# Optimization experiments

Hardware: AMD Instinct MI355X
Metric: run time of the kernel (lower is better)

Reference implementation:

```python
import jax, jax.numpy as jnp
import numpy as np
from jax import lax

B, S, C_IN, D, H, P, W, DFF, K = 32, 4096, 32, 256, 8, 24, 64, 512, 5
DH = D // H
EPS = 1e-5


def _make_starts():
    stride = max(1, W // 2)
    idx = list(range(0, max(S - W + 1, 1), stride))
    if len(idx) == 0 or idx[-1] != S - W:
        if S - W >= 0:
            idx.append(S - W)
    return np.asarray(idx)

STARTS = _make_starts()                      # [M]
WIDX = STARTS[:, None] + np.arange(W)        # [M, W] patch gather indices


def setup_inputs() -> dict:
    key = jax.random.key(0)
    ks = jax.random.split(key, 24)
    r = lambda i, shape, s=0.02: (jax.random.normal(ks[i], shape, jnp.float32) * s)
    return {
        "x": jax.random.normal(ks[0], (B, S, C_IN), jnp.float32),
        "last_close_unused": jnp.zeros((B,), jnp.float32),
        "dw_w": r(1, (C_IN, 1, K), 0.2),      # depthwise conv kernel
        "pw_w": r(2, (D, C_IN), 0.1),         # pointwise conv (1x1)
        "bn_g": jnp.ones((D,), jnp.float32),
        "bn_b": jnp.zeros((D,), jnp.float32),
        "lg_Wq": r(3, (D, D)), "lg_Wk": r(4, (D, D)),
        "lg_Wv": r(5, (D, D)), "lg_Wo": r(6, (D, D)),
        "dec_Qd": r(7, (P, D), 1.0 / np.sqrt(D)),
        "dec_Wq": r(8, (D, D)), "dec_Wk": r(9, (D, D)),
        "dec_Wv": r(10, (D, D)), "dec_Wo": r(11, (D, D)),
        "ff1_w": r(12, (DFF, D)), "ff1_b": jnp.zeros((DFF,), jnp.float32),
        "ff2_w": r(13, (D, DFF)), "ff2_b": jnp.zeros((D,), jnp.float32),
        "out_w": r(14, (1, D)), "out_b": jnp.zeros((1,), jnp.float32),
        "gate_logits": jnp.tile(jnp.array([0.2, 0.4, 0.4], jnp.float32), (P, 1)),
    }


def _ln(x):
    m = x.mean(-1, keepdims=True)
    v = ((x - m) ** 2).mean(-1, keepdims=True)
    return (x - m) / jnp.sqrt(v + EPS)


def _split(t):  # [B, L, D] -> [B, H, L, DH]
    return t.reshape(t.shape[0], -1, H, DH).transpose(0, 2, 1, 3)


def _mha(Q, KV, Wq, Wk, Wv, scale):
    q = _split(Q @ Wq.T)
    k = _split(KV @ Wk.T)
    v = _split(KV @ Wv.T)
    attn = jax.nn.softmax(jnp.einsum('bhqd,bhkd->bhqk', q, k) * scale, axis=-1)
    o = jnp.einsum('bhqk,bhkd->bhqd', attn, v)
    o = o.transpose(0, 2, 1, 3).reshape(Q.shape[0], -1, D)
    return o, attn


def reference(x, last_close_unused, dw_w, pw_w, bn_g, bn_b,
              lg_Wq, lg_Wk, lg_Wv, lg_Wo,
              dec_Qd, dec_Wq, dec_Wk, dec_Wv, dec_Wo,
              ff1_w, ff1_b, ff2_w, ff2_b, out_w, out_b, gate_logits):
    # --- DepthwisePointwise front-end ---
    xt = jnp.transpose(x, (0, 2, 1))                         # [B, C, S]
    z = lax.conv_general_dilated(xt, dw_w, (1,), [(K // 2, K // 2)],
                                 dimension_numbers=('NCH', 'OIH', 'NCH'),
                                 feature_group_count=C_IN)
    z = jnp.einsum('dc,bcs->bds', pw_w, z)                   # pointwise 1x1
    z = jax.nn.gelu(z, approximate=False)
    m = z.mean((0, 2), keepdims=True)                        # BatchNorm1d (batch stats)
    v = ((z - m) ** 2).mean((0, 2), keepdims=True)
    z = (z - m) / jnp.sqrt(v + EPS) * bn_g[None, :, None] + bn_b[None, :, None]
    z = jnp.transpose(z, (0, 2, 1))                          # [B, S, D]

    # --- LocalGlobalAttention: patch-mean queries over full sequence K/V ---
    Q = z[:, WIDX].mean(axis=2)                              # [B, M, D]
    scale = 1.0 / np.sqrt(DH)
    o, attn_g = _mha(Q, z, lg_Wq, lg_Wk, lg_Wv, scale)
    Hh = _ln(o @ lg_Wo.T + Q)                                # [B, M, D]

    # --- CrossDecoder: learned queries ---
    Qd = jnp.broadcast_to(dec_Qd[None], (B, P, D))
    o2, attn_d = _mha(Qd, Hh, dec_Wq, dec_Wk, dec_Wv, scale)
    z2 = _ln(o2 @ dec_Wo.T + Qd)
    u = jax.nn.gelu(z2 @ ff1_w.T + ff1_b, approximate=False)
    u = _ln(u @ ff2_w.T + ff2_b + z2)
    y_global = (u @ out_w.T + out_b)[..., 0]                 # [B, P]

    # --- Gated combine: residual=0, local=global ---
    g = jax.nn.softmax(gate_logits, axis=-1)                 # [P, 3]
    y = g[:, 1][None, :] * y_global + g[:, 2][None, :] * y_global
    return (y, attn_g, attn_d)
```

## Files before the change

kernel.cpp:

```cpp
#include <hip/hip_runtime.h>
#include <hip/hip_bf16.h>
#include <cmath>

typedef unsigned short u16;
typedef __attribute__((ext_vector_type(4))) float f32x4;
typedef __attribute__((ext_vector_type(8))) short s16x8;

__device__ __forceinline__ float b2f(u16 u) { return __uint_as_float(((unsigned)u) << 16); }
__device__ __forceinline__ u16 f2b(float f) {
    unsigned u = __float_as_uint(f);
    unsigned r = (u + 0x7fffu + ((u >> 16) & 1u)) >> 16;
    return (u16)r;
}
__device__ __forceinline__ float gelu_f(float x) {
    float t = x * (0.7978845608f + 0.0356774081f * x * x);
    float e = exp2f(2.885390082f * t);
    return 0.5f * x * (1.0f + (e - 1.0f) / (e + 1.0f));
}

#define FOLD 0.25503590f

__global__ __launch_bounds__(256) void prep0_k(const float* __restrict__ pw_w,
        const float* __restrict__ lg_Wq, const float* __restrict__ lg_Wo,
        const float* __restrict__ dec_Wk, const float* __restrict__ dec_Wv,
        const float* __restrict__ dec_Wo, const float* __restrict__ ff1_w,
        const float* __restrict__ ff2_w,
        u16* __restrict__ pwb, u16* __restrict__ Wq_b, u16* __restrict__ Wo_b,
        u16* __restrict__ Wk2_b, u16* __restrict__ Wv2_b, u16* __restrict__ Wo2b,
        u16* __restrict__ ff1b, u16* __restrict__ ff2b)
{
    int idx = blockIdx.x * 256 + threadIdx.x;
    if (idx < 327680) {
        int which = idx >> 16, r = idx & 65535;
        const float* srcs[5] = {lg_Wq, lg_Wo, dec_Wk, dec_Wv, dec_Wo};
        u16* dsts[5] = {Wq_b, Wo_b, Wk2_b, Wv2_b, Wo2b};
        dsts[which][r] = f2b(srcs[which][r]);
    } else if (idx < 458752) {
        int r = idx - 327680;
        ff1b[r] = f2b(ff1_w[r]);
    } else if (idx < 589824) {
        int r = idx - 458752;
        ff2b[r] = f2b(ff2_w[r]);
    } else {
        int r = idx - 589824;
        pwb[r] = f2b(pw_w[r]);
    }
}

__global__ __launch_bounds__(256) void dwpw_k(const float* __restrict__ x,
        const float* __restrict__ dw_w, const u16* __restrict__ pwb,
        u16* __restrict__ zp, float* __restrict__ csum, float* __restrict__ csum2)
{
    __shared__ float xs[68][33];
    __shared__ __align__(16) u16 As[64][40];
    const int t = threadIdx.x;
    const int b = blockIdx.x >> 6, s0 = (blockIdx.x & 63) << 6;
    const int r0 = blockIdx.x * 64;
    const int lane = t & 63, w = t >> 6;
    const int l16 = lane & 15, hi = lane >> 4;

    for (int idx = t; idx < 68 * 32; idx += 256) {
        int row = idx >> 5, c = idx & 31;
        int sg = s0 - 2 + row;
        xs[row][c] = (sg >= 0 && sg < 4096) ? x[((size_t)b * 4096 + sg) * 32 + c] : 0.0f;
    }
    const int cc = t & 31;
    float wv[5];
    #pragma unroll
    for (int k = 0; k < 5; ++k) wv[k] = dw_w[cc * 5 + k];
    __syncthreads();
    #pragma unroll
    for (int i = 0; i < 8; ++i) {
        int sl = (t + i * 256) >> 5;
        float acc = 0;
        #pragma unroll
        for (int k = 0; k < 5; ++k) acc += xs[sl + k][cc] * wv[k];
        As[sl][cc] = f2b(acc);
    }
    __syncthreads();

    const int n0 = w * 64;
    f32x4 zero = {0, 0, 0, 0};
    s16x8 bf[4];
    #pragma unroll
    for (int ni = 0; ni < 4; ++ni)
        bf[ni] = *(const s16x8*)(pwb + (n0 + ni * 16 + l16) * 32 + hi * 8);

    float cl[4] = {0,0,0,0}, ch[4] = {0,0,0,0};
    float ql[4] = {0,0,0,0}, qh[4] = {0,0,0,0};

    #pragma unroll
    for (int mi = 0; mi < 4; ++mi) {
        s16x8 af = *(const s16x8*)&As[mi * 16 + l16][hi * 8];
        #pragma unroll
        for (int ni = 0; ni < 4; ++ni) {
            f32x4 acc = __builtin_amdgcn_mfma_f32_16x16x32_bf16(af, bf[ni], zero, 0, 0, 0);
            int col = n0 + ni * 16 + l16;
            int rowb = r0 + mi * 16 + hi * 4;
            #pragma unroll
            for (int r = 0; r < 4; ++r) {
                float e = gelu_f(acc[r]);
                zp[(size_t)(rowb + r) * 256 + col] = f2b(e);
                if (mi < 2) { cl[ni] += e; ql[ni] += e * e; }
                else        { ch[ni] += e; qh[ni] += e * e; }
            }
        }
    }
    #pragma unroll
    for (int ni = 0; ni < 4; ++ni) {
        #pragma unroll
        for (int m = 16; m <= 32; m <<= 1) {
            cl[ni] += __shfl_xor(cl[ni], m);
            ch[ni] += __shfl_xor(ch[ni], m);
            ql[ni] += __shfl_xor(ql[ni], m);
            qh[ni] += __shfl_xor(qh[ni], m);
        }
        if (lane < 16) {
            int col = n0 + ni * 16 + lane;
            size_t bc = (size_t)(r0 >> 5);
            csum [bc * 256 + col]       = cl[ni];
            csum [(bc + 1) * 256 + col] = ch[ni];
            csum2[bc * 256 + col]       = ql[ni];
            csum2[(bc + 1) * 256 + col] = qh[ni];
        }
    }
}

__global__ __launch_bounds__(256) void stats2_k(const float* __restrict__ csum,
        const float* __restrict__ csum2, float* __restrict__ statp)
{
    int j = blockIdx.x, t = threadIdx.x;
    float s1 = 0, s2 = 0;
    for (int i = 0; i < 64; ++i) {
        s1 += csum [(size_t)(j * 64 + i) * 256 + t];
        s2 += csum2[(size_t)(j * 64 + i) * 256 + t];
    }
    statp[j * 512 + t] = s1;
    statp[j * 512 + 256 + t] = s2;
}

__global__ __launch_bounds__(256) void prep1_k(const float* __restrict__ statp,
        const float* __restrict__ bn_g, const float* __restrict__ bn_b,
        const float* __restrict__ gate_logits,
        float* __restrict__ a_ws, float* __restrict__ c_ws, float* __restrict__ coef)
{
    int t = threadIdx.x;
    float s1 = 0, s2 = 0;
    for (int j = 0; j < 64; ++j) {
        s1 += statp[j * 512 + t];
        s2 += statp[j * 512 + 256 + t];
    }
    const float invN = 1.0f / 131072.0f;
    float mean = s1 * invN;
    float var = s2 * invN - mean * mean;
    float av = bn_g[t] * rsqrtf(var + 1e-5f);
    a_ws[t] = av;
    c_ws[t] = bn_b[t] - mean * av;
    if (t < 24) {
        float g0 = gate_logits[t * 3], g1 = gate_logits[t * 3 + 1], g2 = gate_logits[t * 3 + 2];
        float mx = fmaxf(g0, fmaxf(g1, g2));
        float e0 = __expf(g0 - mx), e1 = __expf(g1 - mx), e2 = __expf(g2 - mx);
        coef[t] = (e1 + e2) / (e0 + e1 + e2);
    }
}

__global__ __launch_bounds__(256) void prepx_k(const float* __restrict__ lg_Wk,
        const float* __restrict__ lg_Wv, const float* __restrict__ a_ws,
        const float* __restrict__ c_ws, const float* __restrict__ dec_Qd,
        const float* __restrict__ dec_Wq, const float* __restrict__ csum,
        const u16* __restrict__ Wq_b,
        u16* __restrict__ Wk_b, u16* __restrict__ Wv_b,
        float* __restrict__ betak, float* __restrict__ betav,
        float* __restrict__ q2, u16* __restrict__ qb)
{
    __shared__ __align__(16) char sm[41728];
    const int bid = blockIdx.x, t = threadIdx.x;
    if (bid < 512) {
        float* red = (float*)sm;
        int which = bid >> 8, row = bid & 255;
        const float* Wsrc = which ? lg_Wv : lg_Wk;
        float wv = Wsrc[row * 256 + t];
        (which ? Wv_b : Wk_b)[row * 256 + t] = f2b(wv * a_ws[t]);
        float v = wv * c_ws[t];
        for (int m = 32; m; m >>= 1) v += __shfl_xor(v, m);
        if ((t & 63) == 0) red[t >> 6] = v;
        __syncthreads();
        if (t == 0) (which ? betav : betak)[row] = red[0] + red[1] + red[2] + red[3];
    } else if (bid < 528) {
        float (*wq)[260] = (float(*)[260])sm;
        float (*qd)[260] = (float(*)[260])(sm + 16640);
        int j = bid - 512;
        for (int idx = t; idx < 4096; idx += 256) {
            int tl = idx >> 8, d = idx & 255;
            wq[tl][d] = dec_Wq[(j * 16 + tl) * 256 + d];
        }
        for (int idx = t; idx < 6144; idx += 256) {
            int p = idx >> 8, d = idx & 255;
            qd[p][d] = dec_Qd[idx];
        }
        __syncthreads();
        for (int o = t; o < 384; o += 256) {
            int p = o >> 4, tl = o & 15;
            float s = 0;
            #pragma unroll 8
            for (int d = 0; d < 256; ++d) s += qd[p][d] * wq[tl][d];
            q2[p * 256 + j * 16 + tl] = s;
        }
    } else {
        u16* As = (u16*)sm;
        float* aa = (float*)(sm + 32768);
        float* ccx = (float*)(sm + 33792);
        const int r0 = (bid - 528) * 64;
        const int lane = t & 63, w = t >> 6;
        const int l16 = lane & 15, hi = lane >> 4;
        aa[t] = a_ws[t] * 0.015625f;
        ccx[t] = c_ws[t];
        __syncthreads();
        #pragma unroll
        for (int i = 0; i < 8; ++i) {
            int c = t + i * 256;
            int row = c >> 5, c16 = c & 31;
            int g = r0 + row, mm = g & 127;
            u16 tmp[8];
            if (mm == 127) {
                #pragma unroll
                for (int j = 0; j < 8; ++j) tmp[j] = 0;
            } else {
                const float* c0p = csum + (size_t)g * 256 + c16 * 8;
                const float* c1p = c0p + 256;
                #pragma unroll
                for (int j = 0; j < 8; ++j) {
                    int d = c16 * 8 + j;
                    tmp[j] = f2b((c0p[j] + c1p[j]) * aa[d] + ccx[d]);
                }
            }
            int boff = (c16 * 16) ^ ((row & 7) << 4);
            *(s16x8*)((char*)As + row * 512 + boff) = *(s16x8*)tmp;
        }
        __syncthreads();
        const int n0 = w * 64;
        f32x4 zero = {0, 0, 0, 0};
        f32x4 acc[4][4];
        #pragma unroll
        for (int mi = 0; mi < 4; ++mi)
            #pragma unroll
            for (int ni = 0; ni < 4; ++ni) acc[mi][ni] = zero;
        #pragma unroll
        for (int kk = 0; kk < 8; ++kk) {
            s16x8 af[4], bf[4];
            #pragma unroll
            for (int mi = 0; mi < 4; ++mi) {
                int row = mi * 16 + l16;
                int boff = (kk * 64 + hi * 16) ^ ((row & 7) << 4);
                af[mi] = *(const s16x8*)((const char*)As + row * 512 + boff);
            }
            #pragma unroll
            for (int ni = 0; ni < 4; ++ni)
                bf[ni] = *(const s16x8*)(Wq_b + (n0 + ni * 16 + l16) * 256 + kk * 32 + hi * 8);
            #pragma unroll
            for (int mi = 0; mi < 4; ++mi)
                #pragma unroll
                for (int ni = 0; ni < 4; ++ni)
                    acc[mi][ni] = __builtin_amdgcn_mfma_f32_16x16x32_bf16(af[mi], bf[ni], acc[mi][ni], 0, 0, 0);
        }
        #pragma unroll
        for (int mi = 0; mi < 4; ++mi)
            #pragma unroll
            for (int ni = 0; ni < 4; ++ni) {
                int col = n0 + ni * 16 + l16;
                int rowb = r0 + mi * 16 + hi * 4;
                #pragma unroll
                for (int r = 0; r < 4; ++r)
                    qb[(size_t)(rowb + r) * 256 + col] = f2b(acc[mi][ni][r] * FOLD);
            }
    }
}

__global__ __launch_bounds__(256) void kv_k(const u16* __restrict__ zp,
        const u16* __restrict__ Wk, const u16* __restrict__ Wv,
        const float* __restrict__ betak, const float* __restrict__ betav,
        u16* __restrict__ kb, u16* __restrict__ vT)
{
    __shared__ __align__(16) char smem[36864];
    const int t = threadIdx.x;
    const int r0 = blockIdx.x * 64;
    const int lane = t & 63, w = t >> 6;
    const int l16 = lane & 15, hi = lane >> 4;

    const u16* Ag = zp + (size_t)r0 * 256;
    #pragma unroll
    for (int i = 0; i < 8; ++i) {
        int c = t + i * 256;
        int row = c >> 5, c16 = c & 31;
        s16x8 v = *(const s16x8*)(Ag + row * 256 + c16 * 8);
        int boff = (c16 * 16) ^ ((row & 7) << 4);
        *(s16x8*)(smem + row * 512 + boff) = v;
    }
    __syncthreads();

    const int n0 = w * 64;
    f32x4 zero = {0, 0, 0, 0};
    f32x4 acc[4][4];
    #pragma unroll
    for (int mi = 0; mi < 4; ++mi)
        #pragma unroll
        for (int ni = 0; ni < 4; ++ni) acc[mi][ni] = zero;

    #pragma unroll
    for (int kk = 0; kk < 8; ++kk) {
        s16x8 af[4], bfk[4];
        #pragma unroll
        for (int mi = 0; mi < 4; ++mi) {
            int row = mi * 16 + l16;
            int boff = (kk * 64 + hi * 16) ^ ((row & 7) << 4);
            af[mi] = *(const s16x8*)(smem + row * 512 + boff);
        }
        #pragma unroll
        for (int ni = 0; ni < 4; ++ni)
            bfk[ni] = *(const s16x8*)(Wk + (n0 + ni * 16 + l16) * 256 + kk * 32 + hi * 8);
        #pragma unroll
        for (int mi = 0; mi < 4; ++mi)
            #pragma unroll
            for (int ni = 0; ni < 4; ++ni)
                acc[mi][ni] = __builtin_amdgcn_mfma_f32_16x16x32_bf16(af[mi], bfk[ni], acc[mi][ni], 0, 0, 0);
    }
    #pragma unroll
    for (int mi = 0; mi < 4; ++mi)
        #pragma unroll
        for (int ni = 0; ni < 4; ++ni) {
            int col = n0 + ni * 16 + l16;
            float bv = betak[col];
            int rowb = r0 + mi * 16 + hi * 4;
            #pragma unroll
            for (int r = 0; r < 4; ++r)
                kb[(size_t)(rowb + r) * 256 + col] = f2b(acc[mi][ni][r] + bv);
        }

    #pragma unroll
    for (int mi = 0; mi < 4; ++mi)
        #pragma unroll
        for (int ni = 0; ni < 4; ++ni) acc[mi][ni] = zero;
    #pragma unroll
    for (int kk = 0; kk < 8; ++kk) {
        s16x8 af[4], bfv[4];
        #pragma unroll
        for (int mi = 0; mi < 4; ++mi) {
            int row = mi * 16 + l16;
            int boff = (kk * 64 + hi * 16) ^ ((row & 7) << 4);
            af[mi] = *(const s16x8*)(smem + row * 512 + boff);
        }
        #pragma unroll
        for (int ni = 0; ni < 4; ++ni)
            bfv[ni] = *(const s16x8*)(Wv + (n0 + ni * 16 + l16) * 256 + kk * 32 + hi * 8);
        #pragma unroll
        for (int mi = 0; mi < 4; ++mi)
            #pragma unroll
            for (int ni = 0; ni < 4; ++ni)
                acc[mi][ni] = __builtin_amdgcn_mfma_f32_16x16x32_bf16(af[mi], bfv[ni], acc[mi][ni], 0, 0, 0);
    }
    __syncthreads();
    #pragma unroll
    for (int mi = 0; mi < 4; ++mi)
        #pragma unroll
        for (int ni = 0; ni < 4; ++ni) {
            int col = n0 + ni * 16 + l16;
            float bv = betav[col];
            int rowb = mi * 16 + hi * 4;
            ushort4 pk;
            pk.x = f2b(acc[mi][ni][0] + bv);
            pk.y = f2b(acc[mi][ni][1] + bv);
            pk.z = f2b(acc[mi][ni][2] + bv);
            pk.w = f2b(acc[mi][ni][3] + bv);
            char* p = smem + col * 144 + ((((rowb >> 3) ^ (col & 7)) & 7) << 4) + ((rowb & 7) << 1);
            *(ushort4*)p = pk;
        }
    __syncthreads();
    const int b = r0 >> 12;
    const int sblk = (r0 & 4095) >> 6;
    u16* vout = vT + (size_t)(b * 8) * 131072 + (size_t)sblk * 2048;
    #pragma unroll
    for (int j = 0; j < 8; ++j) {
        int gid = j * 256 + t;
        int col = gid >> 3, oct = gid & 7;
        const char* p = smem + col * 144 + (((oct ^ (col & 7)) & 7) << 4);
        s16x8 v = *(const s16x8*)p;
        int h = col >> 5, dh = col & 31;
        *(s16x8*)(vout + (size_t)h * 131072 + dh * 64 + oct * 8) = v;
    }
}

template<int MODE>
__global__ __launch_bounds__(256) void gemm_g(const u16* __restrict__ A,
        const u16* __restrict__ W, const float* __restrict__ bias,
        void* __restrict__ Cout, int K, int ntn)
{
    __shared__ u16 As[64 * 256];
    const int t = threadIdx.x;
    const int rt = blockIdx.x / ntn, nt = blockIdx.x % ntn;
    const int r0 = rt * 64, N = ntn * 256;
    const int lane = t & 63, w = t >> 6;
    const int l16 = lane & 15, hi = lane >> 4;

    const u16* Ag = A + (size_t)r0 * K;
    const int n0 = w * 64;
    f32x4 zero = {0, 0, 0, 0};
    f32x4 acc[4][4];
    #pragma unroll
    for (int mi = 0; mi < 4; ++mi)
        #pragma unroll
        for (int ni = 0; ni < 4; ++ni) acc[mi][ni] = zero;

    for (int kc = 0; kc < K; kc += 256) {
        if (kc) __syncthreads();
        #pragma unroll
        for (int i = 0; i < 8; ++i) {
            int c = t + i * 256;
            int row = c >> 5, c16 = c & 31;
            s16x8 v = *(const s16x8*)(Ag + (size_t)row * K + kc + c16 * 8);
            int boff = (c16 * 16) ^ ((row & 7) << 4);
            *(s16x8*)((char*)As + row * 512 + boff) = v;
        }
        __syncthreads();
        #pragma unroll
        for (int kk = 0; kk < 8; ++kk) {
            s16x8 af[4], bf[4];
            #pragma unroll
            for (int mi = 0; mi < 4; ++mi) {
                int row = mi * 16 + l16;
                int boff = (kk * 64 + hi * 16) ^ ((row & 7) << 4);
                af[mi] = *(const s16x8*)((const char*)As + row * 512 + boff);
            }
            #pragma unroll
            for (int ni = 0; ni < 4; ++ni) {
                int j = nt * 256 + n0 + ni * 16 + l16;
                bf[ni] = *(const s16x8*)(W + (size_t)j * K + kc + kk * 32 + hi * 8);
            }
            #pragma unroll
            for (int mi = 0; mi < 4; ++mi)
                #pragma unroll
                for (int ni = 0; ni < 4; ++ni)
                    acc[mi][ni] = __builtin_amdgcn_mfma_f32_16x16x32_bf16(af[mi], bf[ni], acc[mi][ni], 0, 0, 0);
        }
    }

    #pragma unroll
    for (int mi = 0; mi < 4; ++mi)
        #pragma unroll
        for (int ni = 0; ni < 4; ++ni) {
            int col = nt * 256 + n0 + ni * 16 + l16;
            float bv = bias ? bias[col] : 0.0f;
            int rowb = r0 + mi * 16 + hi * 4;
            #pragma unroll
            for (int r = 0; r < 4; ++r) {
                float v = acc[mi][ni][r] + bv;
                if (MODE == 0)      ((u16*)Cout)[(size_t)(rowb + r) * N + col] = f2b(v);
                else if (MODE == 1) ((float*)Cout)[(size_t)(rowb + r) * N + col] = v;
                else                ((u16*)Cout)[(size_t)(rowb + r) * N + col] = f2b(gelu_f(v));
            }
        }
}

__global__ __launch_bounds__(256) void gemm_dual(const u16* __restrict__ A,
        const u16* __restrict__ W0, const u16* __restrict__ W1,
        u16* __restrict__ C0, u16* __restrict__ C1)
{
    __shared__ u16 As[64 * 256];
    const int t = threadIdx.x;
    const int which = blockIdx.x >> 6;
    const int r0 = (blockIdx.x & 63) * 64;
    const u16* W = which ? W1 : W0;
    u16* C = which ? C1 : C0;
    const int lane = t & 63, w = t >> 6;
    const int l16 = lane & 15, hi = lane >> 4;

    const u16* Ag = A + (size_t)r0 * 256;
    #pragma unroll
    for (int i = 0; i < 8; ++i) {
        int c = t + i * 256;
        int row = c >> 5, c16 = c & 31;
        s16x8 v = *(const s16x8*)(Ag + row * 256 + c16 * 8);
        int boff = (c16 * 16) ^ ((row & 7) << 4);
        *(s16x8*)((char*)As + row * 512 + boff) = v;
    }
    __syncthreads();

    const int n0 = w * 64;
    f32x4 zero = {0, 0, 0, 0};
    f32x4 acc[4][4];
    #pragma unroll
    for (int mi = 0; mi < 4; ++mi)
        #pragma unroll
        for (int ni = 0; ni < 4; ++ni) acc[mi][ni] = zero;

    #pragma unroll
    for (int kk = 0; kk < 8; ++kk) {
        s16x8 af[4], bf[4];
        #pragma unroll
        for (int mi = 0; mi < 4; ++mi) {
            int row = mi * 16 + l16;
            int boff = (kk * 64 + hi * 16) ^ ((row & 7) << 4);
            af[mi] = *(const s16x8*)((const char*)As + row * 512 + boff);
        }
        #pragma unroll
        for (int ni = 0; ni < 4; ++ni)
            bf[ni] = *(const s16x8*)(W + (n0 + ni * 16 + l16) * 256 + kk * 32 + hi * 8);
        #pragma unroll
        for (int mi = 0; mi < 4; ++mi)
            #pragma unroll
            for (int ni = 0; ni < 4; ++ni)
                acc[mi][ni] = __builtin_amdgcn_mfma_f32_16x16x32_bf16(af[mi], bf[ni], acc[mi][ni], 0, 0, 0);
    }
    #pragma unroll
    for (int mi = 0; mi < 4; ++mi)
        #pragma unroll
        for (int ni = 0; ni < 4; ++ni) {
            int col = n0 + ni * 16 + l16;
            int rowb = r0 + mi * 16 + hi * 4;
            #pragma unroll
            for (int r = 0; r < 4; ++r)
                C[(size_t)(rowb + r) * 256 + col] = f2b(acc[mi][ni][r]);
        }
}

__global__ __launch_bounds__(512) void attn_k(const u16* __restrict__ qb,
        const u16* __restrict__ kb, const u16* __restrict__ vT,
        u16* __restrict__ ob, float* __restrict__ attn_out)
{
    const int b = blockIdx.x >> 3, h = blockIdx.x & 7;
    const int t = threadIdx.x, w = t >> 6, lane = t & 63;
    const int l16 = lane & 15, hi = lane >> 4;

    __shared__ u16 p_lds[8][16][48];
    __shared__ float buf[8][16][68];

    s16x8 qf = *(const s16x8*)(qb + ((size_t)(b * 128 + w * 16 + l16)) * 256 + h * 32 + hi * 8);
    const u16* kbase = kb + (size_t)b * 4096 * 256 + h * 32 + hi * 8;
    const u16* vbase = vT + (size_t)(b * 8 + h) * 131072 + hi * 8;

    float dacc[4] = {0, 0, 0, 0};
    f32x4 zero = {0, 0, 0, 0};
    f32x4 oacc[2]; oacc[0] = zero; oacc[1] = zero;

    s16x8 kf0 = *(const s16x8*)(kbase + (size_t)l16 * 256);
    s16x8 kf1 = *(const s16x8*)(kbase + (size_t)(16 + l16) * 256);
    s16x8 vf0 = *(const s16x8*)(vbase + l16 * 64);
    s16x8 vf1 = *(const s16x8*)(vbase + (16 + l16) * 64);

    for (int s0 = 0; s0 < 4096; s0 += 32) {
        s16x8 k0 = kf0, k1 = kf1, v0 = vf0, v1 = vf1;
        int sn = s0 + 32;
        if (sn < 4096) {
            kf0 = *(const s16x8*)(kbase + (size_t)(sn + l16) * 256);
            kf1 = *(const s16x8*)(kbase + (size_t)(sn + 16 + l16) * 256);
            vf0 = *(const s16x8*)(vbase + (sn >> 6) * 2048 + l16 * 64 + (sn & 63));
            vf1 = *(const s16x8*)(vbase + (sn >> 6) * 2048 + (16 + l16) * 64 + (sn & 63));
        }
        f32x4 lg0 = __builtin_amdgcn_mfma_f32_16x16x32_bf16(qf, k0, zero, 0, 0, 0);
        f32x4 lg1 = __builtin_amdgcn_mfma_f32_16x16x32_bf16(qf, k1, zero, 0, 0, 0);
        #pragma unroll
        for (int r = 0; r < 4; ++r) {
            float e0 = exp2f(lg0[r]);
            float e1 = exp2f(lg1[r]);
            dacc[r] += e0 + e1;
            p_lds[w][hi * 4 + r][l16] = f2b(e0);
            p_lds[w][hi * 4 + r][16 + l16] = f2b(e1);
        }
        s16x8 pf = *(const s16x8*)(&p_lds[w][l16][hi * 8]);
        oacc[0] = __builtin_amdgcn_mfma_f32_16x16x32_bf16(pf, v0, oacc[0], 0, 0, 0);
        oacc[1] = __builtin_amdgcn_mfma_f32_16x16x32_bf16(pf, v1, oacc[1], 0, 0, 0);
    }

    #pragma unroll
    for (int m = 1; m <= 8; m <<= 1) {
        #pragma unroll
        for (int r = 0; r < 4; ++r) dacc[r] += __shfl_xor(dacc[r], m);
    }
    float rinv[4];
    #pragma unroll
    for (int r = 0; r < 4; ++r) rinv[r] = 1.0f / dacc[r];

    #pragma unroll
    for (int vi = 0; vi < 2; ++vi)
        #pragma unroll
        for (int r = 0; r < 4; ++r) {
            int mg = w * 16 + hi * 4 + r;
            ob[(size_t)(b * 128 + mg) * 256 + h * 32 + vi * 16 + l16] = f2b(oacc[vi][r] * rinv[r]);
        }

    float* ab = attn_out + (size_t)(b * 8 + h) * 127 * 4096;
    const int srow = lane >> 4;
    const int scol = (lane & 15) * 4;

    for (int s0 = 0; s0 < 4096; s0 += 64) {
        #pragma unroll
        for (int kk = 0; kk < 4; ++kk) {
            int sg = s0 + kk * 16 + l16;
            s16x8 kf = *(const s16x8*)(kbase + (size_t)sg * 256);
            f32x4 lg = __builtin_amdgcn_mfma_f32_16x16x32_bf16(qf, kf, zero, 0, 0, 0);
            #pragma unroll
            for (int r = 0; r < 4; ++r)
                buf[w][hi * 4 + r][kk * 16 + l16] = exp2f(lg[r]) * rinv[r];
        }
        #pragma unroll
        for (int rb = 0; rb < 4; ++rb) {
            int row = rb * 4 + srow;
            int mg = w * 16 + row;
            f32x4 v = *(const f32x4*)&buf[w][row][scol];
            if (mg < 127)
                *(f32x4*)(ab + (size_t)mg * 4096 + s0 + scol) = v;
        }
    }
}

__global__ __launch_bounds__(256) void gemm_lnhh(const u16* __restrict__ A,
        const u16* __restrict__ W, const float* __restrict__ csum,
        const float* __restrict__ a_ws, const float* __restrict__ c_ws,
        u16* __restrict__ Hb)
{
    __shared__ __align__(16) char sm[67584];
    __shared__ float aa[256], cc2[256];
    float (*Cs)[264] = (float(*)[264])sm;
    const int t = threadIdx.x;
    const int r0 = blockIdx.x * 64;
    const int lane = t & 63, w = t >> 6;
    const int l16 = lane & 15, hi = lane >> 4;

    aa[t] = a_ws[t] * 0.015625f;
    cc2[t] = c_ws[t];

    const u16* Ag = A + (size_t)r0 * 256;
    #pragma unroll
    for (int i = 0; i < 8; ++i) {
        int c = t + i * 256;
        int row = c >> 5, c16 = c & 31;
        s16x8 v = *(const s16x8*)(Ag + row * 256 + c16 * 8);
        int boff = (c16 * 16) ^ ((row & 7) << 4);
        *(s16x8*)(sm + row * 512 + boff) = v;
    }
    __syncthreads();

    const int n0 = w * 64;
    f32x4 zero = {0, 0, 0, 0};
    f32x4 acc[4][4];
    #pragma unroll
    for (int mi = 0; mi < 4; ++mi)
        #pragma unroll
        for (int ni = 0; ni < 4; ++ni) acc[mi][ni] = zero;
    #pragma unroll
    for (int kk = 0; kk < 8; ++kk) {
        s16x8 af[4], bf[4];
        #pragma unroll
        for (int mi = 0; mi < 4; ++mi) {
            int row = mi * 16 + l16;
            int boff = (kk * 64 + hi * 16) ^ ((row & 7) << 4);
            af[mi] = *(const s16x8*)(sm + row * 512 + boff);
        }
        #pragma unroll
        for (int ni = 0; ni < 4; ++ni)
            bf[ni] = *(const s16x8*)(W + (n0 + ni * 16 + l16) * 256 + kk * 32 + hi * 8);
        #pragma unroll
        for (int mi = 0; mi < 4; ++mi)
            #pragma unroll
            for (int ni = 0; ni < 4; ++ni)
                acc[mi][ni] = __builtin_amdgcn_mfma_f32_16x16x32_bf16(af[mi], bf[ni], acc[mi][ni], 0, 0, 0);
    }
    __syncthreads();
    #pragma unroll
    for (int mi = 0; mi < 4; ++mi)
        #pragma unroll
        for (int ni = 0; ni < 4; ++ni) {
            int col = n0 + ni * 16 + l16;
            int rowb = mi * 16 + hi * 4;
            #pragma unroll
            for (int r = 0; r < 4; ++r)
                Cs[rowb + r][col] = acc[mi][ni][r];
        }
    __syncthreads();
    for (int pass = 0; pass < 16; ++pass) {
        int row = pass * 4 + w;
        int g = r0 + row, mm = g & 127;
        float v[4];
        #pragma unroll
        for (int j = 0; j < 4; ++j) {
            int d = lane + j * 64;
            float qv = 0.0f;
            if (mm != 127)
                qv = (csum[(size_t)g * 256 + d] + csum[(size_t)(g + 1) * 256 + d]) * aa[d] + cc2[d];
            v[j] = Cs[row][d] + qv;
        }
        float s = v[0] + v[1] + v[2] + v[3];
        for (int m = 32; m; m >>= 1) s += __shfl_xor(s, m);
        float mean = s * (1.0f / 256.0f);
        float q = 0;
        #pragma unroll
        for (int j = 0; j < 4; ++j) { float d_ = v[j] - mean; q += d_ * d_; }
        for (int m = 32; m; m >>= 1) q += __shfl_xor(q, m);
        float rs = rsqrtf(q * (1.0f / 256.0f) + 1e-5f);
        #pragma unroll
        for (int j = 0; j < 4; ++j)
            Hb[(size_t)g * 256 + lane + j * 64] = f2b((v[j] - mean) * rs);
    }
}

__global__ __launch_bounds__(256) void dec_attn_k(const float* __restrict__ q2,
        const u16* __restrict__ k2b, const u16* __restrict__ v2b,
        float* __restrict__ attn_d, u16* __restrict__ o2b)
{
    __shared__ float qs2[24 * 32];
    __shared__ float ks[128][33];
    __shared__ float vs[128][33];
    __shared__ float lg2[24 * 128];
    __shared__ float sinv[24];
    int bid = blockIdx.x, b = bid >> 3, h = bid & 7;
    int t = threadIdx.x;
    const float scale = 0.17677669529663687f;
    for (int idx = t; idx < 4096; idx += 256) {
        int row = idx >> 5, c = idx & 31;
        ks[row][c] = b2f(k2b[((size_t)(b * 128 + row)) * 256 + h * 32 + c]);
        vs[row][c] = b2f(v2b[((size_t)(b * 128 + row)) * 256 + h * 32 + c]);
    }
    for (int idx = t; idx < 768; idx += 256) {
        int p = idx >> 5, i = idx & 31;
        qs2[idx] = q2[p * 256 + h * 32 + i];
    }
    __syncthreads();
    for (int idx = t; idx < 3048; idx += 256) {
        int p = idx / 127, m = idx - p * 127;
        float s = 0;
        #pragma unroll 8
        for (int i = 0; i < 32; ++i) s += qs2[p * 32 + i] * ks[m][i];
        lg2[p * 128 + m] = __expf(s * scale);
    }
    __syncthreads();
    if (t < 24) {
        float s = 0;
        for (int m = 0; m < 127; ++m) s += lg2[t * 128 + m];
        sinv[t] = 1.0f / s;
    }
    __syncthreads();
    float* ad = attn_d + (size_t)bid * 24 * 127;
    for (int idx = t; idx < 3048; idx += 256) {
        int p = idx / 127, m = idx - p * 127;
        float av = lg2[p * 128 + m] * sinv[p];
        lg2[p * 128 + m] = av;
        ad[idx] = av;
    }
    __syncthreads();
    for (int idx = t; idx < 768; idx += 256) {
        int p = idx >> 5, dh = idx & 31;
        float s = 0;
        for (int m = 0; m < 127; ++m)
            s += lg2[p * 128 + m] * vs[m][dh];
        o2b[((size_t)(b * 24 + p)) * 256 + h * 32 + dh] = f2b(s);
    }
}

__global__ __launch_bounds__(256) void gemm_ln3(const u16* __restrict__ A,
        const u16* __restrict__ W, const float* __restrict__ dec_Qd,
        float* __restrict__ z2f, u16* __restrict__ z2b)
{
    __shared__ __align__(16) char sm[67584];
    float (*Cs)[264] = (float(*)[264])sm;
    const int t = threadIdx.x;
    const int r0 = blockIdx.x * 64;
    const int lane = t & 63, w = t >> 6;
    const int l16 = lane & 15, hi = lane >> 4;

    const u16* Ag = A + (size_t)r0 * 256;
    #pragma unroll
    for (int i = 0; i < 8; ++i) {
        int c = t + i * 256;
        int row = c >> 5, c16 = c & 31;
        s16x8 v = *(const s16x8*)(Ag + row * 256 + c16 * 8);
        int boff = (c16 * 16) ^ ((row & 7) << 4);
        *(s16x8*)(sm + row * 512 + boff) = v;
    }
    __syncthreads();

    const int n0 = w * 64;
    f32x4 zero = {0, 0, 0, 0};
    f32x4 acc[4][4];
    #pragma unroll
    for (int mi = 0; mi < 4; ++mi)
        #pragma unroll
        for (int ni = 0; ni < 4; ++ni) acc[mi][ni] = zero;
    #pragma unroll
    for (int kk = 0; kk < 8; ++kk) {
        s16x8 af[4], bf[4];
        #pragma unroll
        for (int mi = 0; mi < 4; ++mi) {
            int row = mi * 16 + l16;
            int boff = (kk * 64 + hi * 16) ^ ((row & 7) << 4);
            af[mi] = *(const s16x8*)(sm + row * 512 + boff);
        }
        #pragma unroll
        for (int ni = 0; ni < 4; ++ni)
            bf[ni] = *(const s16x8*)(W + (n0 + ni * 16 + l16) * 256 + kk * 32 + hi * 8);
        #pragma unroll
        for (int mi = 0; mi < 4; ++mi)
            #pragma unroll
            for (int ni = 0; ni < 4; ++ni)
                acc[mi][ni] = __builtin_amdgcn_mfma_f32_16x16x32_bf16(af[mi], bf[ni], acc[mi][ni], 0, 0, 0);
    }
    __syncthreads();
    #pragma unroll
    for (int mi = 0; mi < 4; ++mi)
        #pragma unroll
        for (int ni = 0; ni < 4; ++ni) {
            int col = n0 + ni * 16 + l16;
            int rowb = mi * 16 + hi * 4;
            #pragma unroll
            for (int r = 0; r < 4; ++r)
                Cs[rowb + r][col] = acc[mi][ni][r];
        }
    __syncthreads();
    for (int pass = 0; pass < 16; ++pass) {
        int row = pass * 4 + w;
        int g = r0 + row, p = g % 24;
        float v[4];
        #pragma unroll
        for (int j = 0; j < 4; ++j) {
            int d = lane + j * 64;
            v[j] = Cs[row][d] + dec_Qd[p * 256 + d];
        }
        float s = v[0] + v[1] + v[2] + v[3];
        for (int m = 32; m; m >>= 1) s += __shfl_xor(s, m);
        float mean = s * (1.0f / 256.0f);
        float q = 0;
        #pragma unroll
        for (int j = 0; j < 4; ++j) { float d_ = v[j] - mean; q += d_ * d_; }
        for (int m = 32; m; m >>= 1) q += __shfl_xor(q, m);
        float rs = rsqrtf(q * (1.0f / 256.0f) + 1e-5f);
        #pragma unroll
        for (int j = 0; j < 4; ++j) {
            float u = (v[j] - mean) * rs;
            z2f[(size_t)g * 256 + lane + j * 64] = u;
            z2b[(size_t)g * 256 + lane + j * 64] = f2b(u);
        }
    }
}

__global__ __launch_bounds__(256) void gemm_ln5(const u16* __restrict__ A,
        const u16* __restrict__ W, const float* __restrict__ bias,
        const float* __restrict__ z2f, const float* __restrict__ out_w,
        const float* __restrict__ out_b, const float* __restrict__ coef,
        float* __restrict__ y)
{
    __shared__ __align__(16) char sm[67584];
    float (*Cs)[264] = (float(*)[264])sm;
    const int t = threadIdx.x;
    const int r0 = blockIdx.x * 64;
    const int lane = t & 63, w = t >> 6;
    const int l16 = lane & 15, hi = lane >> 4;
    const int K = 512;

    const u16* Ag = A + (size_t)r0 * K;
    const int n0 = w * 64;
    f32x4 zero = {0, 0, 0, 0};
    f32x4 acc[4][4];
    #pragma unroll
    for (int mi = 0; mi < 4; ++mi)
        #pragma unroll
        for (int ni = 0; ni < 4; ++ni) acc[mi][ni] = zero;

    for (int kc = 0; kc < K; kc += 256) {
        if (kc) __syncthreads();
        #pragma unroll
        for (int i = 0; i < 8; ++i) {
            int c = t + i * 256;
            int row = c >> 5, c16 = c & 31;
            s16x8 v = *(const s16x8*)(Ag + (size_t)row * K + kc + c16 * 8);
            int boff = (c16 * 16) ^ ((row & 7) << 4);
            *(s16x8*)(sm + row * 512 + boff) = v;
        }
        __syncthreads();
        #pragma unroll
        for (int kk = 0; kk < 8; ++kk) {
            s16x8 af[4], bf[4];
            #pragma unroll
            for (int mi = 0; mi < 4; ++mi) {
                int row = mi * 16 + l16;
                int boff = (kk * 64 + hi * 16) ^ ((row & 7) << 4);
                af[mi] = *(const s16x8*)(sm + row * 512 + boff);
            }
            #pragma unroll
            for (int ni = 0; ni < 4; ++ni)
                bf[ni] = *(const s16x8*)(W + (size_t)(n0 + ni * 16 + l16) * K + kc + kk * 32 + hi * 8);
            #pragma unroll
            for (int mi = 0; mi < 4; ++mi)
                #pragma unroll
                for (int ni = 0; ni < 4; ++ni)
                    acc[mi][ni] = __builtin_amdgcn_mfma_f32_16x16x32_bf16(af[mi], bf[ni], acc[mi][ni], 0, 0, 0);
        }
    }
    __syncthreads();
    #pragma unroll
    for (int mi = 0; mi < 4; ++mi)
        #pragma unroll
        for (int ni = 0; ni < 4; ++ni) {
            int col = n0 + ni * 16 + l16;
            int rowb = mi * 16 + hi * 4;
            #pragma unroll
            for (int r = 0; r < 4; ++r)
                Cs[rowb + r][col] = acc[mi][ni][r];
        }
    __syncthreads();
    for (int pass = 0; pass < 16; ++pass) {
        int row = pass * 4 + w;
        int g = r0 + row, p = g % 24;
        float v[4];
        #pragma unroll
        for (int j = 0; j < 4; ++j) {
            int d = lane + j * 64;
            v[j] = Cs[row][d] + bias[d] + z2f[(size_t)g * 256 + d];
        }
        float s = v[0] + v[1] + v[2] + v[3];
        for (int m = 32; m; m >>= 1) s += __shfl_xor(s, m);
        float mean = s * (1.0f / 256.0f);
        float q = 0;
        #pragma unroll
        for (int j = 0; j < 4; ++j) { float d_ = v[j] - mean; q += d_ * d_; }
        for (int m = 32; m; m >>= 1) q += __shfl_xor(q, m);
        float rs = rsqrtf(q * (1.0f / 256.0f) + 1e-5f);
        float yp = 0;
        #pragma unroll
        for (int j = 0; j < 4; ++j)
            yp += (v[j] - mean) * rs * out_w[lane + j * 64];
        for (int m = 32; m; m >>= 1) yp += __shfl_xor(yp, m);
        if (lane == 0)
            y[g] = coef[p] * (yp + out_b[0]);
    }
}

extern "C" void kernel_launch(void* const* d_in, const int* in_sizes, int n_in,
                              void* d_out, int out_size, void* d_ws, size_t ws_size,
                              hipStream_t stream)
{
    const float* x        = (const float*)d_in[0];
    const float* dw_w     = (const float*)d_in[2];
    const float* pw_w     = (const float*)d_in[3];
    const float* bn_g     = (const float*)d_in[4];
    const float* bn_b     = (const float*)d_in[5];
    const float* lg_Wq    = (const float*)d_in[6];
    const float* lg_Wk    = (const float*)d_in[7];
    const float* lg_Wv    = (const float*)d_in[8];
    const float* lg_Wo    = (const float*)d_in[9];
    const float* dec_Qd   = (const float*)d_in[10];
    const float* dec_Wq   = (const float*)d_in[11];
    const float* dec_Wk   = (const float*)d_in[12];
    const float* dec_Wv   = (const float*)d_in[13];
    const float* dec_Wo   = (const float*)d_in[14];
    const float* ff1_w    = (const float*)d_in[15];
    const float* ff1_b    = (const float*)d_in[16];
    const float* ff2_w    = (const float*)d_in[17];
    const float* ff2_b    = (const float*)d_in[18];
    const float* out_w    = (const float*)d_in[19];
    const float* out_b    = (const float*)d_in[20];
    const float* gate_lg  = (const float*)d_in[21];

    char* ws = (char*)d_ws;
    size_t off = 0;
    auto alloc = [&](size_t bytes) -> void* {
        void* p = ws + off;
        off = (off + bytes + 255) & ~(size_t)255;
        return p;
    };
    u16*   zp    = (u16*)  alloc(67108864);
    u16*   kb    = (u16*)  alloc(67108864);
    u16*   vT    = (u16*)  alloc(67108864);
    float* csum  = (float*)alloc(4194304);
    float* csum2 = (float*)alloc(4194304);
    u16*   qb    = (u16*)  alloc(2097152);
    u16*   ob    = (u16*)  alloc(2097152);
    u16*   Hb    = (u16*)  alloc(2097152);
    u16*   k2b   = (u16*)  alloc(2097152);
    u16*   v2b   = (u16*)  alloc(2097152);
    u16*   o2b   = (u16*)  alloc(393216);
    float* z2f   = (float*)alloc(786432);
    u16*   z2b   = (u16*)  alloc(393216);
    u16*   u1b   = (u16*)  alloc(786432);
    float* q2    = (float*)alloc(24576);
    float* statp = (float*)alloc(131072);
    float* a_ws  = (float*)alloc(1024);
    float* c_ws  = (float*)alloc(1024);
    float* betak = (float*)alloc(1024);
    float* betav = (float*)alloc(1024);
    float* coef  = (float*)alloc(256);
    u16*   pwb   = (u16*)  alloc(16384);
    u16*   Wk_b  = (u16*)  alloc(131072);
    u16*   Wv_b  = (u16*)  alloc(131072);
    u16*   Wq_b  = (u16*)  alloc(131072);
    u16*   Wo_b  = (u16*)  alloc(131072);
    u16*   Wk2_b = (u16*)  alloc(131072);
    u16*   Wv2_b = (u16*)  alloc(131072);
    u16*   Wo2b  = (u16*)  alloc(131072);
    u16*   ff1b  = (u16*)  alloc(262144);
    u16*   ff2b  = (u16*)  alloc(262144);

    float* y_out  = (float*)d_out;
    float* attn_g = y_out + 768;
    float* attn_d = attn_g + (size_t)32 * 8 * 127 * 4096;

    prep0_k<<<2336, 256, 0, stream>>>(pw_w, lg_Wq, lg_Wo, dec_Wk, dec_Wv, dec_Wo, ff1_w, ff2_w,
                                      pwb, Wq_b, Wo_b, Wk2_b, Wv2_b, Wo2b, ff1b, ff2b);
    dwpw_k<<<2048, 256, 0, stream>>>(x, dw_w, pwb, zp, csum, csum2);
    stats2_k<<<64, 256, 0, stream>>>(csum, csum2, statp);
    prep1_k<<<1, 256, 0, stream>>>(statp, bn_g, bn_b, gate_lg, a_ws, c_ws, coef);
    prepx_k<<<592, 256, 0, stream>>>(lg_Wk, lg_Wv, a_ws, c_ws, dec_Qd, dec_Wq, csum, Wq_b,
                                     Wk_b, Wv_b, betak, betav, q2, qb);
    kv_k<<<2048, 256, 0, stream>>>(zp, Wk_b, Wv_b, betak, betav, kb, vT);
    attn_k<<<256, 512, 0, stream>>>(qb, kb, vT, ob, attn_g);
    gemm_lnhh<<<64, 256, 0, stream>>>(ob, Wo_b, csum, a_ws, c_ws, Hb);
    gemm_dual<<<128, 256, 0, stream>>>(Hb, Wk2_b, Wv2_b, k2b, v2b);
    dec_attn_k<<<256, 256, 0, stream>>>(q2, k2b, v2b, attn_d, o2b);
    gemm_ln3<<<12, 256, 0, stream>>>(o2b, Wo2b, dec_Qd, z2f, z2b);
    gemm_g<2><<<24, 256, 0, stream>>>(z2b, ff1b, ff1_b, u1b, 256, 2);
    gemm_ln5<<<12, 256, 0, stream>>>(u1b, ff2b, ff2_b, z2f, out_w, out_b, coef, y_out);
}
```

Measured before the change: 579.9 us.

## Split attention key range across two waves per query group with LDS reduction

```diff
diff --git a/kernel.cpp b/kernel.cpp
--- a/kernel.cpp
+++ b/kernel.cpp
@@ -522,18 +522,19 @@
         }
 }
 
-__global__ __launch_bounds__(512) void attn_k(const u16* __restrict__ qb,
+__global__ __launch_bounds__(1024) void attn_k(const u16* __restrict__ qb,
         const u16* __restrict__ kb, const u16* __restrict__ vT,
         u16* __restrict__ ob, float* __restrict__ attn_out)
 {
+    __shared__ __align__(16) char sm[36864];
     const int b = blockIdx.x >> 3, h = blockIdx.x & 7;
     const int t = threadIdx.x, w = t >> 6, lane = t & 63;
+    const int qg = w >> 1, sh = w & 1;
     const int l16 = lane & 15, hi = lane >> 4;
 
-    __shared__ u16 p_lds[8][16][48];
-    __shared__ float buf[8][16][68];
-
-    s16x8 qf = *(const s16x8*)(qb + ((size_t)(b * 128 + w * 16 + l16)) * 256 + h * 32 + hi * 8);
+    u16* p_lds = (u16*)sm + w * 768;
+
+    s16x8 qf = *(const s16x8*)(qb + ((size_t)(b * 128 + qg * 16 + l16)) * 256 + h * 32 + hi * 8);
     const u16* kbase = kb + (size_t)b * 4096 * 256 + h * 32 + hi * 8;
     const u16* vbase = vT + (size_t)(b * 8 + h) * 131072 + hi * 8;
 
@@ -541,15 +542,16 @@
     f32x4 zero = {0, 0, 0, 0};
     f32x4 oacc[2]; oacc[0] = zero; oacc[1] = zero;
 
-    s16x8 kf0 = *(const s16x8*)(kbase + (size_t)l16 * 256);
-    s16x8 kf1 = *(const s16x8*)(kbase + (size_t)(16 + l16) * 256);
-    s16x8 vf0 = *(const s16x8*)(vbase + l16 * 64);
-    s16x8 vf1 = *(const s16x8*)(vbase + (16 + l16) * 64);
-
-    for (int s0 = 0; s0 < 4096; s0 += 32) {
+    const int sbeg = sh * 2048, send = sbeg + 2048;
+    s16x8 kf0 = *(const s16x8*)(kbase + (size_t)(sbeg + l16) * 256);
+    s16x8 kf1 = *(const s16x8*)(kbase + (size_t)(sbeg + 16 + l16) * 256);
+    s16x8 vf0 = *(const s16x8*)(vbase + (sbeg >> 6) * 2048 + l16 * 64 + (sbeg & 63));
+    s16x8 vf1 = *(const s16x8*)(vbase + (sbeg >> 6) * 2048 + (16 + l16) * 64 + (sbeg & 63));
+
+    for (int s0 = sbeg; s0 < send; s0 += 32) {
         s16x8 k0 = kf0, k1 = kf1, v0 = vf0, v1 = vf1;
         int sn = s0 + 32;
-        if (sn < 4096) {
+        if (sn < send) {
             kf0 = *(const s16x8*)(kbase + (size_t)(sn + l16) * 256);
             kf1 = *(const s16x8*)(kbase + (size_t)(sn + 16 + l16) * 256);
             vf0 = *(const s16x8*)(vbase + (sn >> 6) * 2048 + l16 * 64 + (sn & 63));
@@ -562,10 +564,10 @@
             float e0 = exp2f(lg0[r]);
             float e1 = exp2f(lg1[r]);
             dacc[r] += e0 + e1;
-            p_lds[w][hi * 4 + r][l16] = f2b(e0);
-            p_lds[w][hi * 4 + r][16 + l16] = f2b(e1);
-        }
-        s16x8 pf = *(const s16x8*)(&p_lds[w][l16][hi * 8]);
+            p_lds[(hi * 4 + r) * 48 + l16] = f2b(e0);
+            p_lds[(hi * 4 + r) * 48 + 16 + l16] = f2b(e1);
+        }
+        s16x8 pf = *(const s16x8*)(p_lds + l16 * 48 + hi * 8);
         oacc[0] = __builtin_amdgcn_mfma_f32_16x16x32_bf16(pf, v0, oacc[0], 0, 0, 0);
         oacc[1] = __builtin_amdgcn_mfma_f32_16x16x32_bf16(pf, v1, oacc[1], 0, 0, 0);
     }
@@ -575,37 +577,57 @@
         #pragma unroll
         for (int r = 0; r < 4; ++r) dacc[r] += __shfl_xor(dacc[r], m);
     }
+
+    __syncthreads();
+    float* op = (float*)sm;
+    float* den_s = (float*)(sm + 32768);
+    #pragma unroll
+    for (int vi = 0; vi < 2; ++vi)
+        #pragma unroll
+        for (int r = 0; r < 4; ++r)
+            op[((w * 16 + hi * 4 + r) * 32) + vi * 16 + l16] = oacc[vi][r];
+    if (l16 == 0) {
+        #pragma unroll
+        for (int r = 0; r < 4; ++r) den_s[w * 16 + hi * 4 + r] = dacc[r];
+    }
+    __syncthreads();
     float rinv[4];
     #pragma unroll
-    for (int r = 0; r < 4; ++r) rinv[r] = 1.0f / dacc[r];
-
-    #pragma unroll
-    for (int vi = 0; vi < 2; ++vi)
-        #pragma unroll
-        for (int r = 0; r < 4; ++r) {
-            int mg = w * 16 + hi * 4 + r;
-            ob[(size_t)(b * 128 + mg) * 256 + h * 32 + vi * 16 + l16] = f2b(oacc[vi][r] * rinv[r]);
-        }
-
+    for (int r = 0; r < 4; ++r)
+        rinv[r] = 1.0f / (dacc[r] + den_s[(w ^ 1) * 16 + hi * 4 + r]);
+
+    if (sh == 0) {
+        #pragma unroll
+        for (int vi = 0; vi < 2; ++vi)
+            #pragma unroll
+            for (int r = 0; r < 4; ++r) {
+                int mg = qg * 16 + hi * 4 + r;
+                float o = oacc[vi][r] + op[(((w ^ 1) * 16 + hi * 4 + r) * 32) + vi * 16 + l16];
+                ob[(size_t)(b * 128 + mg) * 256 + h * 32 + vi * 16 + l16] = f2b(o * rinv[r]);
+            }
+    }
+    __syncthreads();
+
+    float* bw = (float*)sm + w * 16 * 36;
     float* ab = attn_out + (size_t)(b * 8 + h) * 127 * 4096;
-    const int srow = lane >> 4;
-    const int scol = (lane & 15) * 4;
-
-    for (int s0 = 0; s0 < 4096; s0 += 64) {
-        #pragma unroll
-        for (int kk = 0; kk < 4; ++kk) {
+    const int srow = lane >> 3;
+    const int scol = (lane & 7) * 4;
+
+    for (int s0 = sbeg; s0 < send; s0 += 32) {
+        #pragma unroll
+        for (int kk = 0; kk < 2; ++kk) {
             int sg = s0 + kk * 16 + l16;
             s16x8 kf = *(const s16x8*)(kbase + (size_t)sg * 256);
             f32x4 lg = __builtin_amdgcn_mfma_f32_16x16x32_bf16(qf, kf, zero, 0, 0, 0);
             #pragma unroll
             for (int r = 0; r < 4; ++r)
-                buf[w][hi * 4 + r][kk * 16 + l16] = exp2f(lg[r]) * rinv[r];
-        }
-        #pragma unroll
-        for (int rb = 0; rb < 4; ++rb) {
-            int row = rb * 4 + srow;
-            int mg = w * 16 + row;
-            f32x4 v = *(const f32x4*)&buf[w][row][scol];
+                bw[(hi * 4 + r) * 36 + kk * 16 + l16] = exp2f(lg[r]) * rinv[r];
+        }
+        #pragma unroll
+        for (int rb = 0; rb < 2; ++rb) {
+            int row = rb * 8 + srow;
+            int mg = qg * 16 + row;
+            f32x4 v = *(const f32x4*)(bw + row * 36 + scol);
             if (mg < 127)
                 *(f32x4*)(ab + (size_t)mg * 4096 + s0 + scol) = v;
         }
@@ -1009,7 +1031,7 @@
     prepx_k<<<592, 256, 0, stream>>>(lg_Wk, lg_Wv, a_ws, c_ws, dec_Qd, dec_Wq, csum, Wq_b,
                                      Wk_b, Wv_b, betak, betav, q2, qb);
     kv_k<<<2048, 256, 0, stream>>>(zp, Wk_b, Wv_b, betak, betav, kb, vT);
-    attn_k<<<256, 512, 0, stream>>>(qb, kb, vT, ob, attn_g);
+    attn_k<<<256, 1024, 0, stream>>>(qb, kb, vT, ob, attn_g);
     gemm_lnhh<<<64, 256, 0, stream>>>(ob, Wo_b, csum, a_ws, c_ws, Hb);
     gemm_dual<<<128, 256, 0, stream>>>(Hb, Wk2_b, Wv2_b, k2b, v2b);
     dec_attn_k<<<256, 256, 0, stream>>>(q2, k2b, v2b, attn_d, o2b);
```

New measurement: 615.5 us. 6.1% more time.
